# Optimization experiments

Measured on AMD Instinct MI355X. Metric: run time of the kernel, lower is better.

## Reference

```python
import jax, jax.numpy as jnp
import numpy as np

B, S, D = 4, 4096, 1024
H = 16
HD = D // H  # 64
EPS = 1e-6


def setup_inputs() -> dict:
    key = jax.random.key(0)
    ks = jax.random.split(key, 7)
    scale = 1.0 / np.sqrt(D)
    return {
        "hidden_states": jax.random.normal(ks[0], (B, S, D), dtype=jnp.float32),
        "Wq": jax.random.normal(ks[1], (D, D), dtype=jnp.float32) * scale,
        "bq": jax.random.normal(ks[2], (D,), dtype=jnp.float32) * 0.02,
        "Wk": jax.random.normal(ks[3], (D, D), dtype=jnp.float32) * scale,
        "bk": jax.random.normal(ks[4], (D,), dtype=jnp.float32) * 0.02,
        "Wv": jax.random.normal(ks[5], (D, D), dtype=jnp.float32) * scale,
        "bv": jax.random.normal(ks[6], (D,), dtype=jnp.float32) * 0.02,
    }


def _heads(x):
    # [B,S,D] -> [B,H,S,HD]
    return x.reshape(B, S, H, HD).transpose(0, 2, 1, 3)


def reference(hidden_states, Wq, bq, Wk, bk, Wv, bv):
    q = _heads(hidden_states @ Wq + bq)
    k = _heads(hidden_states @ Wk + bk)
    v = _heads(hidden_states @ Wv + bv)
    # elu+1 feature maps
    q_feat = jax.nn.elu(q) + 1.0
    k_feat = jax.nn.elu(k) + 1.0
    # kv: [B,H,HD,HD]; k_sum: [B,H,HD]
    kv = jnp.einsum("bhsd,bhse->bhde", k_feat, v)
    k_sum = k_feat.sum(axis=2)
    numerator = jnp.einsum("bhsd,bhde->bhse", q_feat, kv)
    denominator = jnp.einsum("bhsd,bhd->bhs", q_feat, k_sum)
    denominator = jnp.maximum(denominator, EPS)
    out = numerator / denominator[..., None]  # [B,H,S,HD]
    return out.transpose(0, 2, 1, 3).reshape(B, S, D)
```

## Files before the change

kernel.cpp:

```cpp
#include <hip/hip_runtime.h>
#include <math.h>

#define BB 4
#define SS 4096
#define DD 1024
#define HH 16
#define HDD 64
#define MM (BB*SS)
#define EPSV 1e-6f

typedef __bf16 bf16x8 __attribute__((ext_vector_type(8)));
typedef float  f32x4  __attribute__((ext_vector_type(4)));
typedef unsigned short ushort_t;

__device__ __forceinline__ float bf2f(unsigned int u16) {
    unsigned int x = u16 << 16;
    return __uint_as_float(x);
}
__device__ __forceinline__ unsigned short f2bf(float f) {
    unsigned int x = __float_as_uint(f);
    unsigned int r = x + 0x7fffu + ((x >> 16) & 1u);
    return (unsigned short)(r >> 16);
}

#define GLDS16(g, l) __builtin_amdgcn_global_load_lds( \
    (const __attribute__((address_space(1))) void*)(g), \
    (__attribute__((address_space(3))) void*)(l), 16, 0, 0)

__global__ void zero_kernel(float* __restrict__ p, int n) {
    int i = blockIdx.x * blockDim.x + threadIdx.x;
    if (i < n) p[i] = 0.0f;
}

__global__ __launch_bounds__(256) void cvt_hs(const float* __restrict__ in,
                                              ushort_t* __restrict__ out) {
    size_t i = ((size_t)blockIdx.x * 256 + threadIdx.x) * 8;
    float4 f0 = *reinterpret_cast<const float4*>(&in[i]);
    float4 f1 = *reinterpret_cast<const float4*>(&in[i + 4]);
    uint4 u;
    u.x = (unsigned)f2bf(f0.x) | ((unsigned)f2bf(f0.y) << 16);
    u.y = (unsigned)f2bf(f0.z) | ((unsigned)f2bf(f0.w) << 16);
    u.z = (unsigned)f2bf(f1.x) | ((unsigned)f2bf(f1.y) << 16);
    u.w = (unsigned)f2bf(f1.z) | ((unsigned)f2bf(f1.w) << 16);
    *reinterpret_cast<uint4*>(&out[i]) = u;
}

__global__ __launch_bounds__(256) void cvt_w(const float* __restrict__ Wq,
                                             const float* __restrict__ Wk,
                                             const float* __restrict__ Wv,
                                             ushort_t* __restrict__ wt) {
    const int z = blockIdx.z;
    const float* __restrict__ W = (z == 0) ? Wq : (z == 1) ? Wk : Wv;
    const int k0 = blockIdx.x * 64;
    const int n0 = blockIdx.y * 64;
    __shared__ float tile[64][65];
    const int t = threadIdx.x;
    {
        const int kk = t >> 2;
        const int c0 = (t & 3) * 16;
#pragma unroll
        for (int c = 0; c < 4; c++) {
            float4 v = *reinterpret_cast<const float4*>(&W[(size_t)(k0 + kk) * DD + n0 + c0 + c * 4]);
            tile[kk][c0 + c * 4 + 0] = v.x;
            tile[kk][c0 + c * 4 + 1] = v.y;
            tile[kk][c0 + c * 4 + 2] = v.z;
            tile[kk][c0 + c * 4 + 3] = v.w;
        }
    }
    __syncthreads();
    const int n = t >> 2;
    const int kc = t & 3;
    unsigned short tmp[16];
#pragma unroll
    for (int jj = 0; jj < 16; jj++) tmp[jj] = f2bf(tile[kc * 16 + jj][n]);
    uint4 u0, u1;
    u0.x = tmp[0] | (tmp[1] << 16);  u0.y = tmp[2] | (tmp[3] << 16);
    u0.z = tmp[4] | (tmp[5] << 16);  u0.w = tmp[6] | (tmp[7] << 16);
    u1.x = tmp[8] | (tmp[9] << 16);  u1.y = tmp[10] | (tmp[11] << 16);
    u1.z = tmp[12] | (tmp[13] << 16); u1.w = tmp[14] | (tmp[15] << 16);
    ushort_t* dst = &wt[((size_t)z << 20) + (size_t)(n0 + n) * DD + k0 + kc * 16];
    *reinterpret_cast<uint4*>(dst) = u0;
    *reinterpret_cast<uint4*>(dst + 8) = u1;
}

__global__ __launch_bounds__(256) void qkv_gemm_bf16(
    const ushort_t* __restrict__ A,
    const ushort_t* __restrict__ Bt,
    const float* __restrict__ bq, const float* __restrict__ bk, const float* __restrict__ bv,
    ushort_t* __restrict__ qf, ushort_t* __restrict__ kf, ushort_t* __restrict__ vf)
{
    const int z = blockIdx.z;
    const ushort_t* __restrict__ Bz = Bt + ((size_t)z << 20);
    const float* __restrict__ bias  = (z == 0) ? bq : (z == 1) ? bk : bv;
    ushort_t* __restrict__ out      = (z == 0) ? qf : (z == 1) ? kf : vf;

    const int n0 = blockIdx.x * 128;
    const int m0 = blockIdx.y * 128;

    __shared__ ushort_t As[128 * 32];
    __shared__ ushort_t Bs[128 * 32];

    const int tid = threadIdx.x;
    const int lane = tid & 63;
    const int w  = tid >> 6;
    const int wr = w >> 1;
    const int wc = w & 1;

    f32x4 acc[4][4];
#pragma unroll
    for (int i = 0; i < 4; i++)
#pragma unroll
        for (int j = 0; j < 4; j++) acc[i][j] = (f32x4){0.f, 0.f, 0.f, 0.f};

    const int lrow = lane >> 2;
    const int lkc  = (lane & 3) * 8;

    const int fr = lane & 15;
    const int fk = (lane >> 4) * 8;

    for (int k0 = 0; k0 < DD; k0 += 32) {
        __syncthreads();
#pragma unroll
        for (int si = 0; si < 2; si++) {
            const int seg = w * 2 + si;
            GLDS16(&A [(size_t)(m0 + seg * 16 + lrow) * DD + k0 + lkc], &As[seg * 512]);
            GLDS16(&Bz[(size_t)(n0 + seg * 16 + lrow) * DD + k0 + lkc], &Bs[seg * 512]);
        }
        __syncthreads();
        bf16x8 a[4], b[4];
#pragma unroll
        for (int i = 0; i < 4; i++)
            a[i] = *reinterpret_cast<const bf16x8*>(&As[(wr * 64 + i * 16 + fr) * 32 + fk]);
#pragma unroll
        for (int j = 0; j < 4; j++)
            b[j] = *reinterpret_cast<const bf16x8*>(&Bs[(wc * 64 + j * 16 + fr) * 32 + fk]);
#pragma unroll
        for (int i = 0; i < 4; i++)
#pragma unroll
            for (int j = 0; j < 4; j++)
                acc[i][j] = __builtin_amdgcn_mfma_f32_16x16x32_bf16(a[i], b[j], acc[i][j], 0, 0, 0);
    }

    const int fq = lane >> 4;
    float bias4[4];
#pragma unroll
    for (int j = 0; j < 4; j++) bias4[j] = bias[n0 + wc * 64 + j * 16 + fr];
    const bool isqk = (z < 2);
#pragma unroll
    for (int i = 0; i < 4; i++) {
#pragma unroll
        for (int r = 0; r < 4; r++) {
            const int m = m0 + wr * 64 + i * 16 + fq * 4 + r;
            const int bI = m >> 12;
            const int s  = m & 4095;
#pragma unroll
            for (int j = 0; j < 4; j++) {
                const int n = n0 + wc * 64 + j * 16 + fr;
                const int h = n >> 6, e = n & 63;
                float c = acc[i][j][r] + bias4[j];
                if (isqk) c = (c > 0.f) ? (c + 1.f) : __expf(c);
                out[((size_t)(bI * HH + h) * SS + s) * HDD + e] = f2bf(c);
            }
        }
    }
}

__global__ __launch_bounds__(256) void kv_ksum2(
    const ushort_t* __restrict__ kf, const ushort_t* __restrict__ vf,
    float* __restrict__ kv, float* __restrict__ ksum)
{
    const int bh = blockIdx.x;
    const int s0 = blockIdx.y * 256;

    __shared__ float kb[16][68];
    __shared__ float vb[16][68];

    const int tid = threadIdx.x;
    const int tx = tid & 15;
    const int ty = tid >> 4;

    float acc[4][4] = {};
    float ks4[4] = {};

    const ushort_t* kbase = kf + (size_t)bh * SS * HDD;
    const ushort_t* vbase = vf + (size_t)bh * SS * HDD;

    for (int s = s0; s < s0 + 256; s += 16) {
        __syncthreads();
        {
            int t = tid;
            const ushort_t* src = kbase;
            float (*dst)[68] = kb;
            if (t >= 128) { t -= 128; src = vbase; dst = vb; }
            const int r = t >> 3;
            const int c = (t & 7) * 8;
            uint4 u = *reinterpret_cast<const uint4*>(&src[(size_t)(s + r) * HDD + c]);
            float4 f0 = make_float4(bf2f(u.x & 0xffff), bf2f(u.x >> 16),
                                    bf2f(u.y & 0xffff), bf2f(u.y >> 16));
            float4 f1 = make_float4(bf2f(u.z & 0xffff), bf2f(u.z >> 16),
                                    bf2f(u.w & 0xffff), bf2f(u.w >> 16));
            *reinterpret_cast<float4*>(&dst[r][c])     = f0;
            *reinterpret_cast<float4*>(&dst[r][c + 4]) = f1;
        }
        __syncthreads();
#pragma unroll
        for (int ss = 0; ss < 16; ss++) {
            float4 a = *reinterpret_cast<const float4*>(&kb[ss][ty * 4]);
            float4 b = *reinterpret_cast<const float4*>(&vb[ss][tx * 4]);
            const float av[4] = {a.x, a.y, a.z, a.w};
            const float bv4[4] = {b.x, b.y, b.z, b.w};
#pragma unroll
            for (int i = 0; i < 4; i++)
#pragma unroll
                for (int j = 0; j < 4; j++)
                    acc[i][j] += av[i] * bv4[j];
            if (tx == 0) {
#pragma unroll
                for (int i = 0; i < 4; i++) ks4[i] += av[i];
            }
        }
    }

    float* kvp = kv + (size_t)bh * HDD * HDD;
#pragma unroll
    for (int i = 0; i < 4; i++)
#pragma unroll
        for (int j = 0; j < 4; j++)
            atomicAdd(&kvp[(ty * 4 + i) * HDD + tx * 4 + j], acc[i][j]);
    if (tx == 0) {
#pragma unroll
        for (int i = 0; i < 4; i++)
            atomicAdd(&ksum[bh * HDD + ty * 4 + i], ks4[i]);
    }
}

__global__ __launch_bounds__(256) void out2(
    const ushort_t* __restrict__ qf, const float* __restrict__ kv,
    const float* __restrict__ ksum, float* __restrict__ outp)
{
    const int bh = blockIdx.x;
    const int s0 = blockIdx.y * 64;
    const int bI = bh >> 4, h = bh & 15;

    __shared__ float kvs[64][64];
    __shared__ float qsT[64][68];
    __shared__ float kss[64];
    __shared__ float denp[64][4];
    __shared__ float dens[64];

    const int tid = threadIdx.x;

    {
        const float* kvg = kv + (size_t)bh * HDD * HDD;
        float* kvf = &kvs[0][0];
#pragma unroll
        for (int it = 0; it < 4; it++) {
            const int i = it * 1024 + tid * 4;
            *reinterpret_cast<float4*>(&kvf[i]) = *reinterpret_cast<const float4*>(&kvg[i]);
        }
        if (tid < 64) kss[tid] = ksum[bh * HDD + tid];
    }
    {
        if (tid < 128) {
            const int r = tid >> 1;
            const int e0 = (tid & 1) * 32;
            const ushort_t* qb = qf + ((size_t)bh * SS + s0 + r) * HDD + e0;
#pragma unroll
            for (int q4 = 0; q4 < 4; q4++) {
                uint4 u = *reinterpret_cast<const uint4*>(&qb[q4 * 8]);
                const int eb = e0 + q4 * 8;
                qsT[eb + 0][r] = bf2f(u.x & 0xffff);
                qsT[eb + 1][r] = bf2f(u.x >> 16);
                qsT[eb + 2][r] = bf2f(u.y & 0xffff);
                qsT[eb + 3][r] = bf2f(u.y >> 16);
                qsT[eb + 4][r] = bf2f(u.z & 0xffff);
                qsT[eb + 5][r] = bf2f(u.z >> 16);
                qsT[eb + 6][r] = bf2f(u.w & 0xffff);
                qsT[eb + 7][r] = bf2f(u.w >> 16);
            }
        }
    }
    __syncthreads();

    {
        const int s = tid >> 2, dq = tid & 3;
        float p = 0.f;
#pragma unroll
        for (int ii = 0; ii < 16; ii++) {
            const int d = dq * 16 + ii;
            p += qsT[d][s] * kss[d];
        }
        denp[s][dq] = p;
    }
    __syncthreads();
    if (tid < 64)
        dens[tid] = fmaxf(denp[tid][0] + denp[tid][1] + denp[tid][2] + denp[tid][3], EPSV);
    __syncthreads();

    const int tx = tid & 15;
    const int ry = tid >> 4;
    float acc[4][4] = {};
    for (int d = 0; d < 64; d++) {
        float4 a = *reinterpret_cast<const float4*>(&qsT[d][ry * 4]);
        float4 b = *reinterpret_cast<const float4*>(&kvs[d][tx * 4]);
        const float av[4] = {a.x, a.y, a.z, a.w};
        const float bv4[4] = {b.x, b.y, b.z, b.w};
#pragma unroll
        for (int i = 0; i < 4; i++)
#pragma unroll
            for (int j = 0; j < 4; j++)
                acc[i][j] += av[i] * bv4[j];
    }

    float* ob = outp + ((size_t)(bI * SS + s0) * DD) + h * HDD;
#pragma unroll
    for (int i = 0; i < 4; i++) {
        const float inv = 1.0f / dens[ry * 4 + i];
        float4 o;
        o.x = acc[i][0] * inv; o.y = acc[i][1] * inv;
        o.z = acc[i][2] * inv; o.w = acc[i][3] * inv;
        *reinterpret_cast<float4*>(&ob[(size_t)(ry * 4 + i) * DD + tx * 4]) = o;
    }
}

extern "C" void kernel_launch(void* const* d_in, const int* in_sizes, int n_in,
                              void* d_out, int out_size, void* d_ws, size_t ws_size,
                              hipStream_t stream) {
    const float* hs = (const float*)d_in[0];
    const float* Wq = (const float*)d_in[1];
    const float* bq = (const float*)d_in[2];
    const float* Wk = (const float*)d_in[3];
    const float* bk = (const float*)d_in[4];
    const float* Wv = (const float*)d_in[5];
    const float* bv = (const float*)d_in[6];
    float* outp = (float*)d_out;

    ushort_t* hs_bf = (ushort_t*)d_ws;
    ushort_t* wt_bf = hs_bf + (size_t)MM * DD;
    ushort_t* qf    = wt_bf + ((size_t)3 << 20);
    float*    kvp   = (float*)(qf + (size_t)MM * DD);
    float*    ksum  = kvp + (size_t)BB * HH * HDD * HDD;
    ushort_t* kf = (ushort_t*)d_out;
    ushort_t* vf = kf + (size_t)MM * DD;

    const int nz = BB * HH * HDD * HDD + BB * HH * HDD;
    hipLaunchKernelGGL(zero_kernel, dim3((nz + 255) / 256), dim3(256), 0, stream, kvp, nz);

    hipLaunchKernelGGL(cvt_hs, dim3((MM * DD) / (256 * 8)), dim3(256), 0, stream, hs, hs_bf);
    hipLaunchKernelGGL(cvt_w, dim3(16, 16, 3), dim3(256), 0, stream, Wq, Wk, Wv, wt_bf);

    dim3 g1(DD / 128, MM / 128, 3);
    hipLaunchKernelGGL(qkv_gemm_bf16, g1, dim3(256), 0, stream,
                       hs_bf, wt_bf, bq, bk, bv, qf, kf, vf);

    hipLaunchKernelGGL(kv_ksum2, dim3(BB * HH, 16), dim3(256), 0, stream, kf, vf, kvp, ksum);

    hipLaunchKernelGGL(out2, dim3(BB * HH, SS / 64), dim3(256), 0, stream, qf, kvp, ksum, outp);
}
```

Before: 371.0 us.

## Move kv and output contractions onto MFMA with transposed K/V and split partials

The QKV GEMM now writes K and V transposed (head-dim major), uses a flat swizzled block index for better L2 locality, and drops the zero-init kernel. The kv/ksum reduction moves from FP32 FMA with atomics to bf16 MFMA over 512-token chunks, writing per-chunk partials that a new finalize kernel sums. The finalize kernel also splits kv into bf16 hi/lo pairs so the output contraction can run on MFMA while keeping near-fp32 accuracy. The aim is to cut ALU and atomic cost in the attention stages, at the price of an extra launch, more workspace, and strided transposed stores from the GEMM epilogue.

```diff
diff --git a/kernel.cpp b/kernel.cpp
--- a/kernel.cpp
+++ b/kernel.cpp
@@ -14,8 +14,7 @@
 typedef unsigned short ushort_t;
 
 __device__ __forceinline__ float bf2f(unsigned int u16) {
-    unsigned int x = u16 << 16;
-    return __uint_as_float(x);
+    return __uint_as_float(u16 << 16);
 }
 __device__ __forceinline__ unsigned short f2bf(float f) {
     unsigned int x = __float_as_uint(f);
@@ -26,11 +25,6 @@
 #define GLDS16(g, l) __builtin_amdgcn_global_load_lds( \
     (const __attribute__((address_space(1))) void*)(g), \
     (__attribute__((address_space(3))) void*)(l), 16, 0, 0)
-
-__global__ void zero_kernel(float* __restrict__ p, int n) {
-    int i = blockIdx.x * blockDim.x + threadIdx.x;
-    if (i < n) p[i] = 0.0f;
-}
 
 __global__ __launch_bounds__(256) void cvt_hs(const float* __restrict__ in,
                                               ushort_t* __restrict__ out) {
@@ -87,15 +81,17 @@
     const ushort_t* __restrict__ A,
     const ushort_t* __restrict__ Bt,
     const float* __restrict__ bq, const float* __restrict__ bk, const float* __restrict__ bv,
-    ushort_t* __restrict__ qf, ushort_t* __restrict__ kf, ushort_t* __restrict__ vf)
+    ushort_t* __restrict__ qf, ushort_t* __restrict__ kt, ushort_t* __restrict__ vt)
 {
-    const int z = blockIdx.z;
+    const int id  = blockIdx.x;
+    const int swz = (id & 7) * 384 + (id >> 3);
+    const int z   = swz >> 10;
+    const int rem = swz & 1023;
+    const int m0  = (rem >> 3) * 128;
+    const int n0  = (rem & 7) * 128;
+
     const ushort_t* __restrict__ Bz = Bt + ((size_t)z << 20);
     const float* __restrict__ bias  = (z == 0) ? bq : (z == 1) ? bk : bv;
-    ushort_t* __restrict__ out      = (z == 0) ? qf : (z == 1) ? kf : vf;
-
-    const int n0 = blockIdx.x * 128;
-    const int m0 = blockIdx.y * 128;
 
     __shared__ ushort_t As[128 * 32];
     __shared__ ushort_t Bs[128 * 32];
@@ -114,7 +110,6 @@
 
     const int lrow = lane >> 2;
     const int lkc  = (lane & 3) * 8;
-
     const int fr = lane & 15;
     const int fk = (lane >> 4) * 8;
 
@@ -145,181 +140,241 @@
     float bias4[4];
 #pragma unroll
     for (int j = 0; j < 4; j++) bias4[j] = bias[n0 + wc * 64 + j * 16 + fr];
-    const bool isqk = (z < 2);
-#pragma unroll
-    for (int i = 0; i < 4; i++) {
-#pragma unroll
-        for (int r = 0; r < 4; r++) {
-            const int m = m0 + wr * 64 + i * 16 + fq * 4 + r;
+
+    if (z == 0) {
+#pragma unroll
+        for (int i = 0; i < 4; i++) {
+#pragma unroll
+            for (int r = 0; r < 4; r++) {
+                const int m = m0 + wr * 64 + i * 16 + fq * 4 + r;
+                const int bI = m >> 12;
+                const int s  = m & 4095;
+#pragma unroll
+                for (int j = 0; j < 4; j++) {
+                    const int n = n0 + wc * 64 + j * 16 + fr;
+                    const int h = n >> 6, e = n & 63;
+                    float c = acc[i][j][r] + bias4[j];
+                    c = (c > 0.f) ? (c + 1.f) : __expf(c);
+                    qf[((size_t)(bI * HH + h) * SS + s) * HDD + e] = f2bf(c);
+                }
+            }
+        }
+    } else {
+        ushort_t* __restrict__ outt = (z == 1) ? kt : vt;
+        const bool isk = (z == 1);
+#pragma unroll
+        for (int i = 0; i < 4; i++) {
+            const int m = m0 + wr * 64 + i * 16 + fq * 4;
             const int bI = m >> 12;
             const int s  = m & 4095;
 #pragma unroll
             for (int j = 0; j < 4; j++) {
                 const int n = n0 + wc * 64 + j * 16 + fr;
                 const int h = n >> 6, e = n & 63;
-                float c = acc[i][j][r] + bias4[j];
-                if (isqk) c = (c > 0.f) ? (c + 1.f) : __expf(c);
-                out[((size_t)(bI * HH + h) * SS + s) * HDD + e] = f2bf(c);
+                ushort4 u;
+                float c0 = acc[i][j][0] + bias4[j];
+                float c1 = acc[i][j][1] + bias4[j];
+                float c2 = acc[i][j][2] + bias4[j];
+                float c3 = acc[i][j][3] + bias4[j];
+                if (isk) {
+                    c0 = (c0 > 0.f) ? (c0 + 1.f) : __expf(c0);
+                    c1 = (c1 > 0.f) ? (c1 + 1.f) : __expf(c1);
+                    c2 = (c2 > 0.f) ? (c2 + 1.f) : __expf(c2);
+                    c3 = (c3 > 0.f) ? (c3 + 1.f) : __expf(c3);
+                }
+                u.x = f2bf(c0); u.y = f2bf(c1); u.z = f2bf(c2); u.w = f2bf(c3);
+                *reinterpret_cast<ushort4*>(
+                    &outt[((size_t)((bI * HH + h) * HDD + e)) * SS + s]) = u;
             }
         }
     }
 }
 
-__global__ __launch_bounds__(256) void kv_ksum2(
-    const ushort_t* __restrict__ kf, const ushort_t* __restrict__ vf,
-    float* __restrict__ kv, float* __restrict__ ksum)
+__global__ __launch_bounds__(256) void kv_mfma(
+    const ushort_t* __restrict__ kt, const ushort_t* __restrict__ vt,
+    float* __restrict__ kv_part, float* __restrict__ ksum_part)
 {
     const int bh = blockIdx.x;
-    const int s0 = blockIdx.y * 256;
-
-    __shared__ float kb[16][68];
-    __shared__ float vb[16][68];
-
+    const int c  = blockIdx.y;
     const int tid = threadIdx.x;
-    const int tx = tid & 15;
-    const int ty = tid >> 4;
-
-    float acc[4][4] = {};
-    float ks4[4] = {};
-
-    const ushort_t* kbase = kf + (size_t)bh * SS * HDD;
-    const ushort_t* vbase = vf + (size_t)bh * SS * HDD;
-
-    for (int s = s0; s < s0 + 256; s += 16) {
-        __syncthreads();
-        {
-            int t = tid;
-            const ushort_t* src = kbase;
-            float (*dst)[68] = kb;
-            if (t >= 128) { t -= 128; src = vbase; dst = vb; }
-            const int r = t >> 3;
-            const int c = (t & 7) * 8;
-            uint4 u = *reinterpret_cast<const uint4*>(&src[(size_t)(s + r) * HDD + c]);
-            float4 f0 = make_float4(bf2f(u.x & 0xffff), bf2f(u.x >> 16),
-                                    bf2f(u.y & 0xffff), bf2f(u.y >> 16));
-            float4 f1 = make_float4(bf2f(u.z & 0xffff), bf2f(u.z >> 16),
-                                    bf2f(u.w & 0xffff), bf2f(u.w >> 16));
-            *reinterpret_cast<float4*>(&dst[r][c])     = f0;
-            *reinterpret_cast<float4*>(&dst[r][c + 4]) = f1;
-        }
-        __syncthreads();
-#pragma unroll
-        for (int ss = 0; ss < 16; ss++) {
-            float4 a = *reinterpret_cast<const float4*>(&kb[ss][ty * 4]);
-            float4 b = *reinterpret_cast<const float4*>(&vb[ss][tx * 4]);
-            const float av[4] = {a.x, a.y, a.z, a.w};
-            const float bv4[4] = {b.x, b.y, b.z, b.w};
-#pragma unroll
-            for (int i = 0; i < 4; i++)
-#pragma unroll
-                for (int j = 0; j < 4; j++)
-                    acc[i][j] += av[i] * bv4[j];
-            if (tx == 0) {
-#pragma unroll
-                for (int i = 0; i < 4; i++) ks4[i] += av[i];
-            }
-        }
-    }
-
-    float* kvp = kv + (size_t)bh * HDD * HDD;
+    const int lane = tid & 63;
+    const int w = tid >> 6;
+    const int fr = lane & 15;
+    const int fq = lane >> 4;
+
+    const size_t base = (size_t)bh * HDD * SS;
+    const int s0 = c * 512;
+
+    bf16x8 ones;
+#pragma unroll
+    for (int x = 0; x < 8; x++) ones[x] = (__bf16)1.0f;
+
+    f32x4 acc[4], ks[4];
+#pragma unroll
+    for (int i = 0; i < 4; i++) { acc[i] = (f32x4){0,0,0,0}; ks[i] = (f32x4){0,0,0,0}; }
+
+#pragma unroll
+    for (int ksi = 0; ksi < 16; ksi++) {
+        const int sc = s0 + ksi * 32 + fq * 8;
+        bf16x8 a[4];
+#pragma unroll
+        for (int i = 0; i < 4; i++)
+            a[i] = *reinterpret_cast<const bf16x8*>(&kt[base + (size_t)(i * 16 + fr) * SS + sc]);
+        bf16x8 b = *reinterpret_cast<const bf16x8*>(&vt[base + (size_t)(w * 16 + fr) * SS + sc]);
+#pragma unroll
+        for (int i = 0; i < 4; i++) {
+            acc[i] = __builtin_amdgcn_mfma_f32_16x16x32_bf16(a[i], b, acc[i], 0, 0, 0);
+            ks[i]  = __builtin_amdgcn_mfma_f32_16x16x32_bf16(a[i], ones, ks[i], 0, 0, 0);
+        }
+    }
+
+    float* kp = kv_part + ((size_t)(bh * 8 + c) << 12);
 #pragma unroll
     for (int i = 0; i < 4; i++)
 #pragma unroll
-        for (int j = 0; j < 4; j++)
-            atomicAdd(&kvp[(ty * 4 + i) * HDD + tx * 4 + j], acc[i][j]);
-    if (tx == 0) {
+        for (int r = 0; r < 4; r++)
+            kp[(i * 16 + fq * 4 + r) * 64 + (w * 16 + fr)] = acc[i][r];
+    if (w == 0 && fr == 0) {
+        float* ksp = ksum_part + (size_t)(bh * 8 + c) * 64;
 #pragma unroll
         for (int i = 0; i < 4; i++)
-            atomicAdd(&ksum[bh * HDD + ty * 4 + i], ks4[i]);
-    }
-}
-
-__global__ __launch_bounds__(256) void out2(
-    const ushort_t* __restrict__ qf, const float* __restrict__ kv,
-    const float* __restrict__ ksum, float* __restrict__ outp)
+#pragma unroll
+            for (int r = 0; r < 4; r++)
+                ksp[i * 16 + fq * 4 + r] = ks[i][r];
+    }
+}
+
+__global__ __launch_bounds__(256) void kv_finalize(
+    const float* __restrict__ kv_part, const float* __restrict__ ksum_part,
+    ushort_t* __restrict__ kvh, ushort_t* __restrict__ kvl, float* __restrict__ ksum)
+{
+    const int bh = blockIdx.x;
+    const int tid = threadIdx.x;
+    __shared__ float lin[4096];
+
+    const float* kp = kv_part + ((size_t)(bh * 8) << 12);
+    float s[16];
+#pragma unroll
+    for (int x = 0; x < 16; x++) s[x] = 0.f;
+#pragma unroll
+    for (int cc = 0; cc < 8; cc++) {
+#pragma unroll
+        for (int g = 0; g < 4; g++) {
+            float4 v = *reinterpret_cast<const float4*>(&kp[((size_t)cc << 12) + tid * 16 + g * 4]);
+            s[g * 4 + 0] += v.x; s[g * 4 + 1] += v.y;
+            s[g * 4 + 2] += v.z; s[g * 4 + 3] += v.w;
+        }
+    }
+#pragma unroll
+    for (int g = 0; g < 4; g++) {
+        float4 v = make_float4(s[g * 4], s[g * 4 + 1], s[g * 4 + 2], s[g * 4 + 3]);
+        *reinterpret_cast<float4*>(&lin[tid * 16 + g * 4]) = v;
+    }
+    if (tid < 64) {
+        float t = 0.f;
+#pragma unroll
+        for (int cc = 0; cc < 8; cc++) t += ksum_part[(size_t)(bh * 8 + cc) * 64 + tid];
+        ksum[bh * 64 + tid] = t;
+    }
+    __syncthreads();
+
+    const int e  = tid >> 2;
+    const int db = tid & 3;
+    ushort_t hi[16], lo[16];
+#pragma unroll
+    for (int dd = 0; dd < 16; dd++) {
+        float v = lin[(db * 16 + dd) * 64 + e];
+        hi[dd] = f2bf(v);
+        lo[dd] = f2bf(v - bf2f(hi[dd]));
+    }
+    ushort_t* ph = &kvh[(size_t)bh * 4096 + e * 64 + db * 16];
+    ushort_t* pl = &kvl[(size_t)bh * 4096 + e * 64 + db * 16];
+#pragma unroll
+    for (int g = 0; g < 2; g++) {
+        uint4 uh, ul;
+        uh.x = hi[g*8+0] | (hi[g*8+1] << 16); uh.y = hi[g*8+2] | (hi[g*8+3] << 16);
+        uh.z = hi[g*8+4] | (hi[g*8+5] << 16); uh.w = hi[g*8+6] | (hi[g*8+7] << 16);
+        ul.x = lo[g*8+0] | (lo[g*8+1] << 16); ul.y = lo[g*8+2] | (lo[g*8+3] << 16);
+        ul.z = lo[g*8+4] | (lo[g*8+5] << 16); ul.w = lo[g*8+6] | (lo[g*8+7] << 16);
+        *reinterpret_cast<uint4*>(ph + g * 8) = uh;
+        *reinterpret_cast<uint4*>(pl + g * 8) = ul;
+    }
+}
+
+__global__ __launch_bounds__(256) void out_mfma(
+    const ushort_t* __restrict__ qf, const ushort_t* __restrict__ kvh,
+    const ushort_t* __restrict__ kvl, const float* __restrict__ ksum,
+    float* __restrict__ outp)
 {
     const int bh = blockIdx.x;
     const int s0 = blockIdx.y * 64;
     const int bI = bh >> 4, h = bh & 15;
-
-    __shared__ float kvs[64][64];
-    __shared__ float qsT[64][68];
+    const int tid = threadIdx.x;
+
     __shared__ float kss[64];
     __shared__ float denp[64][4];
     __shared__ float dens[64];
 
-    const int tid = threadIdx.x;
+    if (tid < 64) kss[tid] = ksum[bh * 64 + tid];
+    __syncthreads();
 
     {
-        const float* kvg = kv + (size_t)bh * HDD * HDD;
-        float* kvf = &kvs[0][0];
-#pragma unroll
-        for (int it = 0; it < 4; it++) {
-            const int i = it * 1024 + tid * 4;
-            *reinterpret_cast<float4*>(&kvf[i]) = *reinterpret_cast<const float4*>(&kvg[i]);
-        }
-        if (tid < 64) kss[tid] = ksum[bh * HDD + tid];
-    }
-    {
-        if (tid < 128) {
-            const int r = tid >> 1;
-            const int e0 = (tid & 1) * 32;
-            const ushort_t* qb = qf + ((size_t)bh * SS + s0 + r) * HDD + e0;
-#pragma unroll
-            for (int q4 = 0; q4 < 4; q4++) {
-                uint4 u = *reinterpret_cast<const uint4*>(&qb[q4 * 8]);
-                const int eb = e0 + q4 * 8;
-                qsT[eb + 0][r] = bf2f(u.x & 0xffff);
-                qsT[eb + 1][r] = bf2f(u.x >> 16);
-                qsT[eb + 2][r] = bf2f(u.y & 0xffff);
-                qsT[eb + 3][r] = bf2f(u.y >> 16);
-                qsT[eb + 4][r] = bf2f(u.z & 0xffff);
-                qsT[eb + 5][r] = bf2f(u.z >> 16);
-                qsT[eb + 6][r] = bf2f(u.w & 0xffff);
-                qsT[eb + 7][r] = bf2f(u.w >> 16);
-            }
-        }
-    }
-    __syncthreads();
-
-    {
-        const int s = tid >> 2, dq = tid & 3;
+        const int sr = tid >> 2, dq = tid & 3;
+        const ushort_t* qp = qf + (size_t)bh * SS * HDD + (size_t)(s0 + sr) * HDD + dq * 16;
+        uint4 u0 = *reinterpret_cast<const uint4*>(qp);
+        uint4 u1 = *reinterpret_cast<const uint4*>(qp + 8);
+        const float* kb = &kss[dq * 16];
         float p = 0.f;
-#pragma unroll
-        for (int ii = 0; ii < 16; ii++) {
-            const int d = dq * 16 + ii;
-            p += qsT[d][s] * kss[d];
-        }
-        denp[s][dq] = p;
+        p += bf2f(u0.x & 0xffff) * kb[0];  p += bf2f(u0.x >> 16) * kb[1];
+        p += bf2f(u0.y & 0xffff) * kb[2];  p += bf2f(u0.y >> 16) * kb[3];
+        p += bf2f(u0.z & 0xffff) * kb[4];  p += bf2f(u0.z >> 16) * kb[5];
+        p += bf2f(u0.w & 0xffff) * kb[6];  p += bf2f(u0.w >> 16) * kb[7];
+        p += bf2f(u1.x & 0xffff) * kb[8];  p += bf2f(u1.x >> 16) * kb[9];
+        p += bf2f(u1.y & 0xffff) * kb[10]; p += bf2f(u1.y >> 16) * kb[11];
+        p += bf2f(u1.z & 0xffff) * kb[12]; p += bf2f(u1.z >> 16) * kb[13];
+        p += bf2f(u1.w & 0xffff) * kb[14]; p += bf2f(u1.w >> 16) * kb[15];
+        denp[sr][dq] = p;
     }
     __syncthreads();
     if (tid < 64)
         dens[tid] = fmaxf(denp[tid][0] + denp[tid][1] + denp[tid][2] + denp[tid][3], EPSV);
     __syncthreads();
 
-    const int tx = tid & 15;
-    const int ry = tid >> 4;
-    float acc[4][4] = {};
-    for (int d = 0; d < 64; d++) {
-        float4 a = *reinterpret_cast<const float4*>(&qsT[d][ry * 4]);
-        float4 b = *reinterpret_cast<const float4*>(&kvs[d][tx * 4]);
-        const float av[4] = {a.x, a.y, a.z, a.w};
-        const float bv4[4] = {b.x, b.y, b.z, b.w};
-#pragma unroll
-        for (int i = 0; i < 4; i++)
-#pragma unroll
-            for (int j = 0; j < 4; j++)
-                acc[i][j] += av[i] * bv4[j];
-    }
-
-    float* ob = outp + ((size_t)(bI * SS + s0) * DD) + h * HDD;
-#pragma unroll
-    for (int i = 0; i < 4; i++) {
-        const float inv = 1.0f / dens[ry * 4 + i];
-        float4 o;
-        o.x = acc[i][0] * inv; o.y = acc[i][1] * inv;
-        o.z = acc[i][2] * inv; o.w = acc[i][3] * inv;
-        *reinterpret_cast<float4*>(&ob[(size_t)(ry * 4 + i) * DD + tx * 4]) = o;
+    const int lane = tid & 63, w = tid >> 6;
+    const int fr = lane & 15, fq = lane >> 4;
+
+    const ushort_t* qb = qf + (size_t)bh * SS * HDD + (size_t)(s0 + w * 16 + fr) * HDD + fq * 8;
+    bf16x8 a0 = *reinterpret_cast<const bf16x8*>(qb);
+    bf16x8 a1 = *reinterpret_cast<const bf16x8*>(qb + 32);
+
+    f32x4 acc[4];
+#pragma unroll
+    for (int j = 0; j < 4; j++) acc[j] = (f32x4){0.f, 0.f, 0.f, 0.f};
+
+    const ushort_t* hb = kvh + ((size_t)bh << 12) + (size_t)fr * HDD + fq * 8;
+    const ushort_t* lb = kvl + ((size_t)bh << 12) + (size_t)fr * HDD + fq * 8;
+#pragma unroll
+    for (int j = 0; j < 4; j++) {
+        const ushort_t* hj = hb + (size_t)j * 16 * HDD;
+        const ushort_t* lj = lb + (size_t)j * 16 * HDD;
+        bf16x8 bh0 = *reinterpret_cast<const bf16x8*>(hj);
+        bf16x8 bh1 = *reinterpret_cast<const bf16x8*>(hj + 32);
+        bf16x8 bl0 = *reinterpret_cast<const bf16x8*>(lj);
+        bf16x8 bl1 = *reinterpret_cast<const bf16x8*>(lj + 32);
+        acc[j] = __builtin_amdgcn_mfma_f32_16x16x32_bf16(a0, bh0, acc[j], 0, 0, 0);
+        acc[j] = __builtin_amdgcn_mfma_f32_16x16x32_bf16(a1, bh1, acc[j], 0, 0, 0);
+        acc[j] = __builtin_amdgcn_mfma_f32_16x16x32_bf16(a0, bl0, acc[j], 0, 0, 0);
+        acc[j] = __builtin_amdgcn_mfma_f32_16x16x32_bf16(a1, bl1, acc[j], 0, 0, 0);
+    }
+
+#pragma unroll
+    for (int r = 0; r < 4; r++) {
+        const int srow = w * 16 + fq * 4 + r;
+        const float inv = 1.0f / dens[srow];
+        float* ob = outp + ((size_t)(bI * SS + s0 + srow)) * DD + h * HDD;
+#pragma unroll
+        for (int j = 0; j < 4; j++)
+            ob[j * 16 + fr] = acc[j][r] * inv;
     }
 }
 
@@ -335,25 +390,26 @@
     const float* bv = (const float*)d_in[6];
     float* outp = (float*)d_out;
 
-    ushort_t* hs_bf = (ushort_t*)d_ws;
-    ushort_t* wt_bf = hs_bf + (size_t)MM * DD;
-    ushort_t* qf    = wt_bf + ((size_t)3 << 20);
-    float*    kvp   = (float*)(qf + (size_t)MM * DD);
-    float*    ksum  = kvp + (size_t)BB * HH * HDD * HDD;
-    ushort_t* kf = (ushort_t*)d_out;
-    ushort_t* vf = kf + (size_t)MM * DD;
-
-    const int nz = BB * HH * HDD * HDD + BB * HH * HDD;
-    hipLaunchKernelGGL(zero_kernel, dim3((nz + 255) / 256), dim3(256), 0, stream, kvp, nz);
+    ushort_t* hs_bf    = (ushort_t*)d_ws;
+    ushort_t* wt_bf    = hs_bf + (size_t)MM * DD;
+    ushort_t* qf       = wt_bf + ((size_t)3 << 20);
+    float*    kv_part  = (float*)(qf + (size_t)MM * DD);
+    float*    ksum_prt = kv_part + ((size_t)64 * 8 << 12);
+    ushort_t* kvh      = (ushort_t*)(ksum_prt + 64 * 8 * 64);
+    ushort_t* kvl      = kvh + (size_t)64 * 4096;
+    float*    ksum     = (float*)(kvl + (size_t)64 * 4096);
+    ushort_t* kt = (ushort_t*)d_out;
+    ushort_t* vt = kt + (size_t)MM * DD;
 
     hipLaunchKernelGGL(cvt_hs, dim3((MM * DD) / (256 * 8)), dim3(256), 0, stream, hs, hs_bf);
     hipLaunchKernelGGL(cvt_w, dim3(16, 16, 3), dim3(256), 0, stream, Wq, Wk, Wv, wt_bf);
 
-    dim3 g1(DD / 128, MM / 128, 3);
-    hipLaunchKernelGGL(qkv_gemm_bf16, g1, dim3(256), 0, stream,
-                       hs_bf, wt_bf, bq, bk, bv, qf, kf, vf);
-
-    hipLaunchKernelGGL(kv_ksum2, dim3(BB * HH, 16), dim3(256), 0, stream, kf, vf, kvp, ksum);
-
-    hipLaunchKernelGGL(out2, dim3(BB * HH, SS / 64), dim3(256), 0, stream, qf, kvp, ksum, outp);
-}
+    hipLaunchKernelGGL(qkv_gemm_bf16, dim3(3072), dim3(256), 0, stream,
+                       hs_bf, wt_bf, bq, bk, bv, qf, kt, vt);
+
+    hipLaunchKernelGGL(kv_mfma, dim3(64, 8), dim3(256), 0, stream, kt, vt, kv_part, ksum_prt);
+    hipLaunchKernelGGL(kv_finalize, dim3(64), dim3(256), 0, stream,
+                       kv_part, ksum_prt, kvh, kvl, ksum);
+    hipLaunchKernelGGL(out_mfma, dim3(64, 64), dim3(256), 0, stream,
+                       qf, kvh, kvl, ksum, outp);
+}
```

Measured after the change: 342.1 us. 7.8% less time.
